# Performance work log

Hardware: AMD Instinct MI355X
Metric: run time of the kernel (lower is better)

## Reference

```python
import jax, jax.numpy as jnp
import numpy as np

B, L, DIN, D, H, NL, DFF = 4, 1024, 64, 512, 8, 3, 2048
DH = D // H
N_RBF = 8
LARGE_NEG, CLAMP = 10000.0, 20.0


def layernorm(x, g, b, eps=1e-5):
    m = x.mean(-1, keepdims=True)
    v = x.var(-1, keepdims=True)
    return (x - m) * jax.lax.rsqrt(v + eps) * g + b


def sinusoidal_pe(length, d):
    pos = np.arange(length, dtype=np.float32)[:, None]
    div = np.exp(np.arange(0, d, 2, dtype=np.float32) * (-np.log(10000.0) / d))
    pe = np.zeros((length, d), dtype=np.float32)
    pe[:, 0::2] = np.sin(pos * div)
    pe[:, 1::2] = np.cos(pos * div)
    return jnp.asarray(pe)


def rbf(v):
    centers = jnp.linspace(0.0, 1.0, N_RBF)
    widths = jnp.full((N_RBF,), 0.2)
    diff = (v[..., None] - centers) / (widths + 1e-6)
    return jnp.exp(-0.5 * diff * diff)


def setup_inputs() -> dict:
    key = jax.random.key(0)
    ks = jax.random.split(key, 40)
    g = lambda k, shape: (jax.random.normal(k, shape) * 0.02).astype(jnp.float32)
    feat_dim = D + 2 + 2 * N_RBF  # base PE + raw(2) + 2 RBFs
    inp = {
        "x": jax.random.normal(ks[0], (B, L, DIN), jnp.float32),
        "lengths": jax.random.randint(ks[1], (B,), L // 2, L + 1),
        "input_delay": jax.random.uniform(ks[2], (B,), jnp.float32),
        "c_local": jax.random.uniform(ks[3], (B, L), jnp.float32).at[:, 0].set(0.0),
        "c_sink": jax.random.uniform(ks[4], (B, L), jnp.float32),
        # input projection
        "in_w": g(ks[5], (D, DIN)), "in_b": jnp.zeros((D,)),
        # delay encoder: Linear(1,D) -> GELU -> Linear(D,D) -> LN
        "de_w1": g(ks[6], (D, 1)), "de_b1": jnp.zeros((D,)),
        "de_w2": g(ks[7], (D, D)), "de_b2": jnp.zeros((D,)),
        "de_ln_g": jnp.ones((D,)), "de_ln_b": jnp.zeros((D,)),
        # corr positional encoding
        "cpe_w": g(ks[8], (D, feat_dim)), "cpe_b": jnp.zeros((D,)),
        "cpe_ln_g": jnp.ones((D,)), "cpe_ln_b": jnp.zeros((D,)),
        "gain": jnp.float32(0.5),
        # bias params
        "alpha": jnp.float32(10.0), "beta": jnp.float32(10.0),
        "floor": jnp.float32(0.1), "gamma": jnp.float32(0.7),
        # per-layer stacks
        "inproj_w": g(ks[9], (NL, 3 * D, D)), "inproj_b": jnp.zeros((NL, 3 * D)),
        "outproj_w": g(ks[10], (NL, D, D)), "outproj_b": jnp.zeros((NL, D)),
        "ln1_g": jnp.ones((NL, D)), "ln1_b": jnp.zeros((NL, D)),
        "ln2_g": jnp.ones((NL, D)), "ln2_b": jnp.zeros((NL, D)),
        "ff_w1": g(ks[11], (NL, DFF, D)), "ff_b1": jnp.zeros((NL, DFF)),
        "ff_w2": g(ks[12], (NL, D, DFF)), "ff_b2": jnp.zeros((NL, D)),
        "out_ln_g": jnp.ones((D,)), "out_ln_b": jnp.zeros((D,)),
    }
    return inp


def _forward(x, input_delay, c_local, c_sink, in_w, in_b, de_w1, de_b1, de_w2, de_b2,
             de_ln_g, de_ln_b, cpe_w, cpe_b, cpe_ln_g, cpe_ln_b, gain, alpha, beta,
             floor, gamma, inproj_w, inproj_b, outproj_w, outproj_b, ln1_g, ln1_b,
             ln2_g, ln2_b, ff_w1, ff_b1, ff_w2, ff_b2, out_ln_g, out_ln_b, lengths):
    Bc, Lc, _ = x.shape
    mask = jnp.arange(Lc)[None, :] >= lengths[:, None]          # [B,L] True=pad

    # input projection
    h = x @ in_w.T + in_b

    # delay feature encoder
    e = input_delay[:, None] @ de_w1.T + de_b1
    e = jax.nn.gelu(e, approximate=False) @ de_w2.T + de_b2
    e = layernorm(e, de_ln_g, de_ln_b)
    h = h + e[:, None, :]

    # corr positional encoding (uses clamped correlations)
    cl = jnp.clip(c_local, 0.0, 1.0)
    cs = jnp.clip(c_sink, 0.0, 1.0)
    pe_base = jnp.broadcast_to(sinusoidal_pe(Lc, D)[None], (Bc, Lc, D))
    z = jnp.concatenate([pe_base, jnp.stack([cl, cs], -1), rbf(cl), rbf(cs)], axis=-1)
    pe = layernorm(z @ cpe_w.T + cpe_b, cpe_ln_g, cpe_ln_b)
    pe = gain * pe
    pe = jnp.where(mask[..., None], 0.0, pe)
    h = h + pe

    # neighbor-correlation attention bias [B,1,L,L] (identical across layers/heads)
    idx = jnp.arange(Lc)
    neigh = jnp.abs(idx[None, :] - idx[:, None]) == 1           # [L,L]
    c_edge = jnp.zeros((Bc, Lc, Lc), x.dtype)
    c_edge = c_edge.at[:, 1:, :-1].set(jnp.broadcast_to(c_local[:, 1:, None], (Bc, Lc - 1, Lc - 1)))
    c_edge = c_edge.at[:, :-1, 1:].set(jnp.broadcast_to(c_local[:, None, 1:], (Bc, Lc - 1, Lc - 1)))
    bias = alpha * jnp.where(neigh[None], c_edge, 0.0)
    bias = jnp.where(mask[:, :, None] | mask[:, None, :], 0.0, bias)

    # sink bias (row 0 only): floor + (1-floor)*(c_sink^gamma)
    c_remap = floor + (1.0 - floor) * jnp.power(cs + 1e-6, gamma)
    sink_row = beta * jnp.where(mask, 0.0, c_remap)             # [B,L]
    attn_bias = bias[:, None].at[:, :, 0, :].add(sink_row[:, None, :])  # [B,1,L,L]

    pad = mask[:, None, None, :].astype(x.dtype)                # [B,1,1,L]
    scale = 1.0 / (DH ** 0.5)

    for i in range(NL):
        hn = layernorm(h, ln1_g[i], ln1_b[i])
        qkv = hn @ inproj_w[i].T + inproj_b[i]                  # [B,L,3D]
        q, k, v = jnp.split(qkv, 3, axis=-1)
        q = q.reshape(Bc, Lc, H, DH).transpose(0, 2, 1, 3)      # [B,H,L,d]
        k = k.reshape(Bc, Lc, H, DH).transpose(0, 2, 1, 3)
        v = v.reshape(Bc, Lc, H, DH).transpose(0, 2, 1, 3)
        scores = jnp.einsum('bhqd,bhkd->bhqk', q, k) * scale + attn_bias
        scores = scores - LARGE_NEG * pad
        scores = scores - scores.max(axis=-1, keepdims=True)
        scores = jnp.clip(scores, -CLAMP, CLAMP)
        attn = jax.nn.softmax(scores, axis=-1)
        o = jnp.einsum('bhqk,bhkd->bhqd', attn, v)
        o = o.transpose(0, 2, 1, 3).reshape(Bc, Lc, D)
        h = h + (o @ outproj_w[i].T + outproj_b[i])
        hn2 = layernorm(h, ln2_g[i], ln2_b[i])
        ff = jax.nn.gelu(hn2 @ ff_w1[i].T + ff_b1[i], approximate=False)
        h = h + (ff @ ff_w2[i].T + ff_b2[i])

    return layernorm(h, out_ln_g, out_ln_b)


def reference(x, lengths, input_delay, c_local, c_sink, in_w, in_b, de_w1, de_b1,
              de_w2, de_b2, de_ln_g, de_ln_b, cpe_w, cpe_b, cpe_ln_g, cpe_ln_b, gain,
              alpha, beta, floor, gamma, inproj_w, inproj_b, outproj_w, outproj_b,
              ln1_g, ln1_b, ln2_g, ln2_b, ff_w1, ff_b1, ff_w2, ff_b2, out_ln_g, out_ln_b):
    return _forward(x, input_delay, c_local, c_sink, in_w, in_b, de_w1, de_b1, de_w2,
                    de_b2, de_ln_g, de_ln_b, cpe_w, cpe_b, cpe_ln_g, cpe_ln_b, gain,
                    alpha, beta, floor, gamma, inproj_w, inproj_b, outproj_w,
                    outproj_b, ln1_g, ln1_b, ln2_g, ln2_b, ff_w1, ff_b1, ff_w2, ff_b2,
                    out_ln_g, out_ln_b, lengths)
```

## Files before the change

kernel.cpp:

```cpp
#include <hip/hip_runtime.h>
#include <math.h>

#define BB 4
#define LL 1024
#define DIN 64
#define DD 512
#define HH 8
#define DH 64
#define NLAYER 3
#define DFF 2048
#define FEAT 530
#define FEATP 576
#define MM 4096

typedef float f32x4 __attribute__((ext_vector_type(4)));
typedef short s16x8 __attribute__((ext_vector_type(8)));

__device__ __forceinline__ unsigned short f2bf(float f) {
    unsigned int u = __float_as_uint(f);
    u += 0x7fffu + ((u >> 16) & 1u);
    return (unsigned short)(u >> 16);
}
__device__ __forceinline__ float bf2f(unsigned short u) {
    return __uint_as_float(((unsigned int)u) << 16);
}
__device__ __forceinline__ float gelu_exact(float x) {
    return 0.5f * x * (1.0f + erff(x * 0.7071067811865475f));
}
__device__ __forceinline__ float wave_reduce_sum(float v) {
    #pragma unroll
    for (int o = 32; o; o >>= 1) v += __shfl_down(v, o);
    return v;
}
__device__ __forceinline__ void gload16(const unsigned short* g, unsigned short* l) {
    __builtin_amdgcn_global_load_lds(
        (const __attribute__((address_space(1))) unsigned int*)g,
        (__attribute__((address_space(3))) unsigned int*)l, 16, 0, 0);
}
__device__ __forceinline__ void cvt16(const float* src, unsigned short* dst) {
    float4 f0 = ((const float4*)src)[0];
    float4 f1 = ((const float4*)src)[1];
    float4 f2 = ((const float4*)src)[2];
    float4 f3 = ((const float4*)src)[3];
    ushort4 o0, o1, o2, o3;
    o0.x = f2bf(f0.x); o0.y = f2bf(f0.y); o0.z = f2bf(f0.z); o0.w = f2bf(f0.w);
    o1.x = f2bf(f1.x); o1.y = f2bf(f1.y); o1.z = f2bf(f1.z); o1.w = f2bf(f1.w);
    o2.x = f2bf(f2.x); o2.y = f2bf(f2.y); o2.z = f2bf(f2.z); o2.w = f2bf(f2.w);
    o3.x = f2bf(f3.x); o3.y = f2bf(f3.y); o3.z = f2bf(f3.z); o3.w = f2bf(f3.w);
    ((ushort4*)dst)[0] = o0;
    ((ushort4*)dst)[1] = o1;
    ((ushort4*)dst)[2] = o2;
    ((ushort4*)dst)[3] = o3;
}

__global__ __launch_bounds__(256) void prologue_kernel(
    const float* __restrict__ c_local, const float* __restrict__ c_sink,
    const int* __restrict__ lengths,
    const float* __restrict__ beta_p, const float* __restrict__ floor_p,
    const float* __restrict__ gamma_p,
    unsigned short* __restrict__ Z, float* __restrict__ srow,
    const float* __restrict__ x, const float* __restrict__ in_w,
    const float* __restrict__ cpe_w,
    unsigned short* __restrict__ x_bf, unsigned short* __restrict__ w_in,
    unsigned short* __restrict__ w_cpe,
    const float* __restrict__ delay, const float* __restrict__ de_w1, const float* __restrict__ de_b1,
    const float* __restrict__ de_w2, const float* __restrict__ de_b2,
    const float* __restrict__ de_lng, const float* __restrict__ de_lnb,
    float* __restrict__ e)
{
    int blk = blockIdx.x;
    int t = threadIdx.x;

    if (blk < LL) {
        int l = blk;
        for (int d = t; d < DD; d += 256) {
            int i = d >> 1;
            float dv = expf((float)(2 * i) * (-0.017988946135618352f));
            float ang = (float)l * dv;
            unsigned short pv = f2bf((d & 1) ? cosf(ang) : sinf(ang));
            #pragma unroll
            for (int bb = 0; bb < 4; ++bb)
                Z[(size_t)(bb * LL + l) * FEATP + d] = pv;
        }
        {
            int bb = t >> 6, j = t & 63;
            float cl = c_local[(size_t)bb * LL + l]; cl = fminf(fmaxf(cl, 0.f), 1.f);
            float cs = c_sink [(size_t)bb * LL + l]; cs = fminf(fmaxf(cs, 0.f), 1.f);
            float v = 0.f;
            if (j == 0) v = cl;
            else if (j == 1) v = cs;
            else if (j < 10)  { float c = (float)(j - 2) * (1.0f / 7.0f);  float df = (cl - c) / 0.200001f; v = expf(-0.5f * df * df); }
            else if (j < 18)  { float c = (float)(j - 10) * (1.0f / 7.0f); float df = (cs - c) / 0.200001f; v = expf(-0.5f * df * df); }
            Z[(size_t)(bb * LL + l) * FEATP + 512 + j] = (j < 18) ? f2bf(v) : 0;
            if (j == 32) {
                float sv = (*beta_p) * ((*floor_p) + (1.f - (*floor_p)) * powf(cs + 1e-6f, *gamma_p));
                srow[bb * LL + l] = (l < lengths[bb]) ? sv : 0.f;
            }
        }
    } else if (blk < LL + 256) {
        const int N0s = MM * DIN;
        const int N1s = N0s + 512 * 64;
        const int NCHs = N1s / 16;
        int vb = blk - LL;
        for (int c = vb * 256 + t; c < NCHs; c += 256 * 256) {
            int i = c * 16;
            if (i < N0s) cvt16(x + i, x_bf + i);
            else         cvt16(in_w + (i - N0s), w_in + (i - N0s));
        }
        for (int j = vb * 256 + t; j < 512 * FEATP; j += 256 * 256) {
            int r = j / FEATP, c2 = j - r * FEATP;
            w_cpe[j] = (c2 < FEAT) ? f2bf(cpe_w[(size_t)r * FEAT + c2]) : 0;
        }
    } else {
        __shared__ float g1[DD];
        __shared__ float red[16];
        int b = blk - (LL + 256);
        float d0 = delay[b];
        g1[t]       = gelu_exact(d0 * de_w1[t]       + de_b1[t]);
        g1[t + 256] = gelu_exact(d0 * de_w1[t + 256] + de_b1[t + 256]);
        __syncthreads();
        float s0 = de_b2[t], s1 = de_b2[t + 256];
        const float* wr0 = de_w2 + (size_t)t * DD;
        const float* wr1 = de_w2 + (size_t)(t + 256) * DD;
        for (int j = 0; j < DD; j += 4) {
            float4 a4 = *(const float4*)(wr0 + j);
            float4 b4 = *(const float4*)(wr1 + j);
            float gj0 = g1[j], gj1 = g1[j+1], gj2 = g1[j+2], gj3 = g1[j+3];
            s0 += a4.x * gj0 + a4.y * gj1 + a4.z * gj2 + a4.w * gj3;
            s1 += b4.x * gj0 + b4.y * gj1 + b4.z * gj2 + b4.w * gj3;
        }
        float s = s0 + s1, ss = s0 * s0 + s1 * s1;
        float rs = wave_reduce_sum(s), rss = wave_reduce_sum(ss);
        int lane = t & 63, w = t >> 6;
        if (lane == 0) { red[w] = rs; red[8 + w] = rss; }
        __syncthreads();
        float mean = 0.f, msq = 0.f;
        #pragma unroll
        for (int i = 0; i < 4; ++i) { mean += red[i]; msq += red[8 + i]; }
        mean *= (1.0f / DD); msq *= (1.0f / DD);
        float rstd = rsqrtf(msq - mean * mean + 1e-5f);
        e[(size_t)b * DD + t]       = (s0 - mean) * rstd * de_lng[t]       + de_lnb[t];
        e[(size_t)b * DD + t + 256] = (s1 - mean) * rstd * de_lng[t + 256] + de_lnb[t + 256];
    }
}

template<int BM, int BN, int FM, int FN, int WGN>
__device__ __forceinline__ void gemm_body(
    const unsigned short* __restrict__ A, const unsigned short* __restrict__ W,
    const float* __restrict__ bias, const float* __restrict__ resid,
    float* __restrict__ outf, unsigned short* __restrict__ outb,
    int M, int N, int K, int mode, int bm, int bn,
    unsigned short* As, unsigned short* Ws)
{
    int t = threadIdx.x;
    int lane = t & 63, wid = t >> 6;
    int wr = wid / WGN, wc = wid % WGN;
    int l15 = lane & 15, lg = lane >> 4;
    int sr = lane >> 3;
    int sc = ((lane & 7) ^ sr) * 8;
    int ph0 = (lg ^ (l15 & 7)) * 8;
    int ph1 = ((lg + 4) ^ (l15 & 7)) * 8;

    f32x4 acc[FM][FN] = {};
    int nk = K >> 6;

    auto stage = [&](int buf, int ks) {
        int kb = ks * 64;
        #pragma unroll
        for (int i = 0; i < BM / 32; ++i) {
            int row = wid * (BM / 4) + i * 8 + sr;
            gload16(A + (size_t)(bm + row) * K + kb + sc, &As[(size_t)buf * BM * 64 + (wid * (BM / 4) + i * 8) * 64]);
        }
        #pragma unroll
        for (int i = 0; i < BN / 32; ++i) {
            int row = wid * (BN / 4) + i * 8 + sr;
            gload16(W + (size_t)(bn + row) * K + kb + sc, &Ws[(size_t)buf * BN * 64 + (wid * (BN / 4) + i * 8) * 64]);
        }
    };

    stage(0, 0);
    __syncthreads();

    int cur = 0;
    for (int ks = 0; ks < nk; ++ks) {
        if (ks + 1 < nk) stage(cur ^ 1, ks + 1);
        s16x8 af0[FM], af1[FM], wf0[FN], wf1[FN];
        #pragma unroll
        for (int mi = 0; mi < FM; ++mi) {
            int row = wr * FM * 16 + mi * 16 + l15;
            af0[mi] = *(const s16x8*)&As[(size_t)cur * BM * 64 + row * 64 + ph0];
            af1[mi] = *(const s16x8*)&As[(size_t)cur * BM * 64 + row * 64 + ph1];
        }
        #pragma unroll
        for (int ni = 0; ni < FN; ++ni) {
            int row = wc * FN * 16 + ni * 16 + l15;
            wf0[ni] = *(const s16x8*)&Ws[(size_t)cur * BN * 64 + row * 64 + ph0];
            wf1[ni] = *(const s16x8*)&Ws[(size_t)cur * BN * 64 + row * 64 + ph1];
        }
        #pragma unroll
        for (int mi = 0; mi < FM; ++mi)
            #pragma unroll
            for (int ni = 0; ni < FN; ++ni) {
                acc[mi][ni] = __builtin_amdgcn_mfma_f32_16x16x32_bf16(af0[mi], wf0[ni], acc[mi][ni], 0, 0, 0);
                acc[mi][ni] = __builtin_amdgcn_mfma_f32_16x16x32_bf16(af1[mi], wf1[ni], acc[mi][ni], 0, 0, 0);
            }
        __syncthreads();
        cur ^= 1;
    }

    int rbase = (lane >> 4) * 4;
    #pragma unroll
    for (int mi = 0; mi < FM; ++mi) {
        #pragma unroll
        for (int ni = 0; ni < FN; ++ni) {
            int n = bn + wc * FN * 16 + ni * 16 + l15;
            float bzc = (mode == 4) ? 0.f : bias[n];
            #pragma unroll
            for (int r2 = 0; r2 < 4; ++r2) {
                int m = bm + wr * FM * 16 + mi * 16 + rbase + r2;
                float v = acc[mi][ni][r2] + ((mode == 4) ? bias[m] : bzc);
                size_t o = (size_t)m * N + n;
                if (mode == 0)      outf[o] = v;
                else if (mode == 1) outb[o] = f2bf(v);
                else if (mode == 2) outf[o] = v + resid[o];
                else if (mode == 3) outb[o] = f2bf(gelu_exact(v));
                else                outb[o] = f2bf(v);
            }
        }
    }
}

template<int BM, int BN, int FM, int FN, int WGN, int MODE>
__global__ __launch_bounds__(256) void gemm_t(
    const unsigned short* __restrict__ A, const unsigned short* __restrict__ W,
    const float* __restrict__ bias, const float* __restrict__ resid,
    float* __restrict__ outf, unsigned short* __restrict__ outb,
    int M, int N, int K)
{
    __shared__ __align__(16) unsigned short As[2 * BM * 64];
    __shared__ __align__(16) unsigned short Ws[2 * BN * 64];
    gemm_body<BM, BN, FM, FN, WGN>(A, W, bias, resid, outf, outb, M, N, K, MODE,
                                   blockIdx.y * BM, blockIdx.x * BN, As, Ws);
}

__global__ __launch_bounds__(256) void gemm_pre_dual(
    const unsigned short* __restrict__ x_bf, const unsigned short* __restrict__ w_in,
    const float* __restrict__ in_b, float* __restrict__ h,
    const unsigned short* __restrict__ Zb, const unsigned short* __restrict__ w_cpe,
    const float* __restrict__ cpe_b, float* __restrict__ cpe_pre,
    const float* __restrict__ inproj_w, const float* __restrict__ outproj_w,
    const float* __restrict__ ff_w1, const float* __restrict__ ff_w2,
    unsigned short* __restrict__ w_inproj, unsigned short* __restrict__ w_outproj,
    unsigned short* __restrict__ w_ff1, unsigned short* __restrict__ w_ff2)
{
    __shared__ __align__(16) unsigned short As[2 * 64 * 64];
    __shared__ __align__(16) unsigned short Ws[2 * 64 * 64];
    int id = blockIdx.x;
    if (id < 512) {
        gemm_body<64, 64, 2, 2, 2>(x_bf, w_in, in_b, nullptr, h, nullptr,
                                   MM, DD, DIN, 0, (id >> 3) * 64, (id & 7) * 64, As, Ws);
    } else if (id < 1024) {
        id -= 512;
        gemm_body<64, 64, 2, 2, 2>(Zb, w_cpe, cpe_b, nullptr, cpe_pre, nullptr,
                                   MM, DD, FEATP, 0, (id >> 3) * 64, (id & 7) * 64, As, Ws);
    } else {
        const int B0 = 3 * 1536 * 512;
        const int B1 = B0 + 3 * 512 * 512;
        const int B2 = B1 + 3 * 2048 * 512;
        const int B3 = B2 + 3 * 512 * 2048;
        const int NCH = B3 / 16;
        int vb = id - 1024;
        int t = threadIdx.x;
        for (int c = vb * 256 + t; c < NCH; c += 1024 * 256) {
            int i = c * 16;
            if (i < B0)      cvt16(inproj_w + i,         w_inproj + i);
            else if (i < B1) cvt16(outproj_w + (i - B0), w_outproj + (i - B0));
            else if (i < B2) cvt16(ff_w1 + (i - B1),     w_ff1 + (i - B1));
            else             cvt16(ff_w2 + (i - B2),     w_ff2 + (i - B2));
        }
    }
}

__global__ __launch_bounds__(256) void gemm_qkv_dual(
    const unsigned short* __restrict__ act1,
    const unsigned short* __restrict__ wqk, const float* __restrict__ qk_bias,
    unsigned short* __restrict__ qkb,
    const unsigned short* __restrict__ wv, const float* __restrict__ v_bias,
    unsigned short* __restrict__ vtb)
{
    __shared__ __align__(16) unsigned short As[2 * 64 * 64];
    __shared__ __align__(16) unsigned short Ws[2 * 64 * 64];
    int id = blockIdx.x;
    if (id < 1024) {
        gemm_body<64, 64, 2, 2, 2>(act1, wqk, qk_bias, nullptr, nullptr, qkb,
                                   MM, 1024, DD, 1, (id >> 4) * 64, (id & 15) * 64, As, Ws);
    } else {
        id -= 1024;
        gemm_body<64, 64, 2, 2, 2>(wv, act1, v_bias, nullptr, nullptr, vtb,
                                   DD, MM, DD, 4, (id >> 6) * 64, (id & 63) * 64, As, Ws);
    }
}

#define SK 72
#define SPB 72
__global__ __launch_bounds__(256) void attn_mfma(
    const unsigned short* __restrict__ qk, const unsigned short* __restrict__ Vt,
    const float* __restrict__ c_local, const float* __restrict__ srow,
    const int* __restrict__ lengths,
    const float* __restrict__ alpha_p,
    unsigned short* __restrict__ o)
{
    __shared__ __align__(16) unsigned short Ks[2][64 * SK];
    __shared__ __align__(16) unsigned short Vts[2][64 * SK];
    __shared__ __align__(16) unsigned short Psb[64 * SPB];

    int id = blockIdx.x;
    int q0 = (id & 15) * 64;
    int hh = (id >> 4) & 7;
    int b  = id >> 7;

    int t  = threadIdx.x;
    int lane = t & 63, w = t >> 6;
    int l15 = lane & 15, lg = lane >> 4;
    int len = lengths[b];
    int nt = (len + 63) >> 6;
    int kt0 = q0 >> 6;
    bool sink_blk = (q0 == 0);
    const float alpha = *alpha_p;

    const unsigned short* qrow = qk + (size_t)(b * LL + q0 + w * 16 + l15) * 1024 + hh * DH;
    s16x8 qf0 = *(const s16x8*)(qrow + lg * 8);
    s16x8 qf1 = *(const s16x8*)(qrow + 32 + lg * 8);
    #pragma unroll
    for (int j = 0; j < 8; ++j) {
        qf0[j] = (short)f2bf(bf2f((unsigned short)qf0[j]) * 0.125f);
        qf1[j] = (short)f2bf(bf2f((unsigned short)qf1[j]) * 0.125f);
    }

    float cm1[4], cp1[4];
    #pragma unroll
    for (int r2 = 0; r2 < 4; ++r2) {
        int qi = q0 + w * 16 + lg * 4 + r2;
        cm1[r2] = 0.f; cp1[r2] = 0.f;
        if (qi >= 1 && qi < len) {
            int src = (qi == 1 || qi == LL - 1) ? qi : qi - 1;
            cm1[r2] = alpha * c_local[(size_t)b * LL + src];
        }
        if (qi + 1 < LL && qi < len)
            cp1[r2] = alpha * c_local[(size_t)b * LL + qi + 1];
    }
    bool need_sink = (sink_blk && w == 0 && lg == 0);

    float m_run[4], l_run[4];
    f32x4 accO[4] = {};
    #pragma unroll
    for (int r2 = 0; r2 < 4; ++r2) { m_run[r2] = -1e30f; l_run[r2] = 0.f; }

    int sr = t >> 3, sc8 = (t & 7) * 8;
    const unsigned short* kbase = qk + (size_t)(b * LL) * 1024 + 512 + hh * DH;
    const unsigned short* vbase = Vt + (size_t)(hh * DH) * MM + b * LL;

    uint4 pk0 = *(const uint4*)(kbase + (size_t)sr * 1024 + sc8);
    uint4 pk1 = *(const uint4*)(kbase + (size_t)(sr + 32) * 1024 + sc8);
    uint4 pv0 = *(const uint4*)(vbase + (size_t)sr * MM + sc8);
    uint4 pv1 = *(const uint4*)(vbase + (size_t)(sr + 32) * MM + sc8);
    *(uint4*)&Ks[0][sr * SK + sc8]         = pk0;
    *(uint4*)&Ks[0][(sr + 32) * SK + sc8]  = pk1;
    *(uint4*)&Vts[0][sr * SK + sc8]        = pv0;
    *(uint4*)&Vts[0][(sr + 32) * SK + sc8] = pv1;
    __syncthreads();

    int cur = 0;
    for (int kt = 0; kt < nt; ++kt) {
        int k0 = kt * 64;
        bool pre = (kt + 1 < nt);
        if (pre) {
            int kn = k0 + 64;
            pk0 = *(const uint4*)(kbase + (size_t)(kn + sr) * 1024 + sc8);
            pk1 = *(const uint4*)(kbase + (size_t)(kn + sr + 32) * 1024 + sc8);
            pv0 = *(const uint4*)(vbase + (size_t)sr * MM + kn + sc8);
            pv1 = *(const uint4*)(vbase + (size_t)(sr + 32) * MM + kn + sc8);
        }

        f32x4 accS[4] = {};
        #pragma unroll
        for (int ct = 0; ct < 4; ++ct) {
            s16x8 kf0 = *(const s16x8*)&Ks[cur][(ct * 16 + l15) * SK + lg * 8];
            s16x8 kf1 = *(const s16x8*)&Ks[cur][(ct * 16 + l15) * SK + 32 + lg * 8];
            accS[ct] = __builtin_amdgcn_mfma_f32_16x16x32_bf16(qf0, kf0, accS[ct], 0, 0, 0);
            accS[ct] = __builtin_amdgcn_mfma_f32_16x16x32_bf16(qf1, kf1, accS[ct], 0, 0, 0);
        }

        float m4[4] = { -1e30f, -1e30f, -1e30f, -1e30f };
        bool slow = sink_blk || (kt >= kt0 - 1 && kt <= kt0 + 1) || (k0 + 64 > len);
        if (!slow) {
            #pragma unroll
            for (int ct = 0; ct < 4; ++ct)
                #pragma unroll
                for (int r2 = 0; r2 < 4; ++r2)
                    m4[r2] = fmaxf(m4[r2], accS[ct][r2]);
        } else if (k0 + 64 <= len) {
            #pragma unroll
            for (int ct = 0; ct < 4; ++ct) {
                int k = k0 + ct * 16 + l15;
                float sink_ct = need_sink ? srow[(size_t)b * LL + k] : 0.f;
                #pragma unroll
                for (int r2 = 0; r2 < 4; ++r2) {
                    int qi = q0 + w * 16 + lg * 4 + r2;
                    float v = accS[ct][r2];
                    if (k == qi - 1) v += cm1[r2];
                    else if (k == qi + 1) v += cp1[r2];
                    if (r2 == 0) v += sink_ct;
                    accS[ct][r2] = v;
                    m4[r2] = fmaxf(m4[r2], v);
                }
            }
        } else {
            #pragma unroll
            for (int ct = 0; ct < 4; ++ct) {
                int k = k0 + ct * 16 + l15;
                bool maskk = (k >= len);
                float sink_ct = need_sink ? srow[(size_t)b * LL + k] : 0.f;
                #pragma unroll
                for (int r2 = 0; r2 < 4; ++r2) {
                    int qi = q0 + w * 16 + lg * 4 + r2;
                    float v = accS[ct][r2];
                    if (k == qi - 1) v += cm1[r2];
                    else if (k == qi + 1 && !maskk) v += cp1[r2];
                    if (r2 == 0) v += sink_ct;
                    if (maskk) v -= 10000.f;
                    accS[ct][r2] = v;
                    m4[r2] = fmaxf(m4[r2], v);
                }
            }
        }

        #pragma unroll
        for (int r2 = 0; r2 < 4; ++r2) {
            #pragma unroll
            for (int msk = 1; msk < 16; msk <<= 1) m4[r2] = fmaxf(m4[r2], __shfl_xor(m4[r2], msk));
            float mnew = fmaxf(m_run[r2], m4[r2]);
            float scl = __expf(m_run[r2] - mnew);
            m_run[r2] = mnew;
            float rowsum = 0.f;
            #pragma unroll
            for (int ct = 0; ct < 4; ++ct) {
                float p = __expf(accS[ct][r2] - mnew);
                rowsum += p;
                Psb[(w * 16 + lg * 4 + r2) * SPB + ct * 16 + l15] = f2bf(p);
            }
            #pragma unroll
            for (int msk = 1; msk < 16; msk <<= 1) rowsum += __shfl_xor(rowsum, msk);
            l_run[r2] = l_run[r2] * scl + rowsum;
            #pragma unroll
            for (int dt = 0; dt < 4; ++dt) accO[dt][r2] *= scl;
        }

        #pragma unroll
        for (int kk = 0; kk < 2; ++kk) {
            s16x8 pf = *(const s16x8*)&Psb[(w * 16 + l15) * SPB + kk * 32 + lg * 8];
            #pragma unroll
            for (int dt = 0; dt < 4; ++dt) {
                s16x8 vf = *(const s16x8*)&Vts[cur][(dt * 16 + l15) * SK + kk * 32 + lg * 8];
                accO[dt] = __builtin_amdgcn_mfma_f32_16x16x32_bf16(pf, vf, accO[dt], 0, 0, 0);
            }
        }

        if (pre) {
            int nxt = cur ^ 1;
            *(uint4*)&Ks[nxt][sr * SK + sc8]         = pk0;
            *(uint4*)&Ks[nxt][(sr + 32) * SK + sc8]  = pk1;
            *(uint4*)&Vts[nxt][sr * SK + sc8]        = pv0;
            *(uint4*)&Vts[nxt][(sr + 32) * SK + sc8] = pv1;
        }
        __syncthreads();
        cur ^= 1;
    }

    #pragma unroll
    for (int r2 = 0; r2 < 4; ++r2) {
        float inv = 1.f / l_run[r2];
        int qi = q0 + w * 16 + lg * 4 + r2;
        #pragma unroll
        for (int dt = 0; dt < 4; ++dt)
            o[(size_t)(b * LL + qi) * DD + hh * DH + dt * 16 + l15] = f2bf(accO[dt][r2] * inv);
    }
}

__global__ __launch_bounds__(256) void embed_ep_kernel(
    const float* __restrict__ cpe_pre, const float* __restrict__ e,
    const int* __restrict__ lengths,
    const float* __restrict__ cpe_g, const float* __restrict__ cpe_lb,
    const float* __restrict__ gain_p, float* __restrict__ h)
{
    int row = blockIdx.x;
    int b = row >> 10, l = row & 1023;
    int t = threadIdx.x;
    __shared__ float red[16];
    const float* cp = cpe_pre + (size_t)row * DD;
    float v0 = cp[t], v1 = cp[t + 256];
    float s = v0 + v1, ss = v0 * v0 + v1 * v1;
    float rs = wave_reduce_sum(s), rss = wave_reduce_sum(ss);
    int lane = t & 63, w = t >> 6;
    if (lane == 0) { red[w] = rs; red[8 + w] = rss; }
    __syncthreads();
    float mean = 0.f, msq = 0.f;
    #pragma unroll
    for (int i = 0; i < 4; ++i) { mean += red[i]; msq += red[8 + i]; }
    mean *= (1.0f / DD); msq *= (1.0f / DD);
    float rstd = rsqrtf(msq - mean * mean + 1e-5f);
    bool maskp = (l >= lengths[b]);
    float gain = *gain_p;
    float pe0 = maskp ? 0.f : gain * ((v0 - mean) * rstd * cpe_g[t] + cpe_lb[t]);
    float pe1 = maskp ? 0.f : gain * ((v1 - mean) * rstd * cpe_g[t + 256] + cpe_lb[t + 256]);
    h[(size_t)row * DD + t]       += e[(size_t)b * DD + t] + pe0;
    h[(size_t)row * DD + t + 256] += e[(size_t)b * DD + t + 256] + pe1;
}

__global__ __launch_bounds__(256) void ln_kernel(
    const float* __restrict__ in, float* __restrict__ out,
    const float* __restrict__ g, const float* __restrict__ bta)
{
    int row = blockIdx.x; int t = threadIdx.x;
    __shared__ float red[16];
    const float* xr = in + (size_t)row * DD;
    float2 v = ((const float2*)xr)[t];
    float s = v.x + v.y, ss = v.x * v.x + v.y * v.y;
    float rs = wave_reduce_sum(s), rss = wave_reduce_sum(ss);
    int lane = t & 63, w = t >> 6;
    if (lane == 0) { red[w] = rs; red[8 + w] = rss; }
    __syncthreads();
    float mean = 0.f, msq = 0.f;
    #pragma unroll
    for (int i = 0; i < 4; ++i) { mean += red[i]; msq += red[8 + i]; }
    mean *= (1.0f / DD); msq *= (1.0f / DD);
    float rstd = rsqrtf(msq - mean * mean + 1e-5f);
    float2 gg = ((const float2*)g)[t], bb = ((const float2*)bta)[t];
    float2 o;
    o.x = (v.x - mean) * rstd * gg.x + bb.x;
    o.y = (v.y - mean) * rstd * gg.y + bb.y;
    ((float2*)(out + (size_t)row * DD))[t] = o;
}

__global__ __launch_bounds__(256) void ln_bf16_kernel(
    const float* __restrict__ in, unsigned short* __restrict__ out,
    const float* __restrict__ g, const float* __restrict__ bta)
{
    int row = blockIdx.x; int t = threadIdx.x;
    __shared__ float red[16];
    const float* xr = in + (size_t)row * DD;
    float2 v = ((const float2*)xr)[t];
    float s = v.x + v.y, ss = v.x * v.x + v.y * v.y;
    float rs = wave_reduce_sum(s), rss = wave_reduce_sum(ss);
    int lane = t & 63, w = t >> 6;
    if (lane == 0) { red[w] = rs; red[8 + w] = rss; }
    __syncthreads();
    float mean = 0.f, msq = 0.f;
    #pragma unroll
    for (int i = 0; i < 4; ++i) { mean += red[i]; msq += red[8 + i]; }
    mean *= (1.0f / DD); msq *= (1.0f / DD);
    float rstd = rsqrtf(msq - mean * mean + 1e-5f);
    float2 gg = ((const float2*)g)[t], bb = ((const float2*)bta)[t];
    ushort2 o;
    o.x = f2bf((v.x - mean) * rstd * gg.x + bb.x);
    o.y = f2bf((v.y - mean) * rstd * gg.y + bb.y);
    ((ushort2*)(out + (size_t)row * DD))[t] = o;
}

extern "C" void kernel_launch(void* const* d_in, const int* in_sizes, int n_in,
                              void* d_out, int out_size, void* d_ws, size_t ws_size,
                              hipStream_t stream)
{
    const float* x          = (const float*)d_in[0];
    const int*   lengths    = (const int*)  d_in[1];
    const float* input_delay= (const float*)d_in[2];
    const float* c_local    = (const float*)d_in[3];
    const float* c_sink     = (const float*)d_in[4];
    const float* in_w       = (const float*)d_in[5];
    const float* in_b       = (const float*)d_in[6];
    const float* de_w1      = (const float*)d_in[7];
    const float* de_b1      = (const float*)d_in[8];
    const float* de_w2      = (const float*)d_in[9];
    const float* de_b2      = (const float*)d_in[10];
    const float* de_ln_g    = (const float*)d_in[11];
    const float* de_ln_b    = (const float*)d_in[12];
    const float* cpe_w      = (const float*)d_in[13];
    const float* cpe_b      = (const float*)d_in[14];
    const float* cpe_ln_g   = (const float*)d_in[15];
    const float* cpe_ln_b   = (const float*)d_in[16];
    const float* gain       = (const float*)d_in[17];
    const float* alpha      = (const float*)d_in[18];
    const float* beta       = (const float*)d_in[19];
    const float* floorp     = (const float*)d_in[20];
    const float* gammap     = (const float*)d_in[21];
    const float* inproj_w   = (const float*)d_in[22];
    const float* inproj_b   = (const float*)d_in[23];
    const float* outproj_w  = (const float*)d_in[24];
    const float* outproj_b  = (const float*)d_in[25];
    const float* ln1_g      = (const float*)d_in[26];
    const float* ln1_b      = (const float*)d_in[27];
    const float* ln2_g      = (const float*)d_in[28];
    const float* ln2_b      = (const float*)d_in[29];
    const float* ff_w1      = (const float*)d_in[30];
    const float* ff_b1      = (const float*)d_in[31];
    const float* ff_w2      = (const float*)d_in[32];
    const float* ff_b2      = (const float*)d_in[33];
    const float* out_ln_g   = (const float*)d_in[34];
    const float* out_ln_b   = (const float*)d_in[35];

    char* base = (char*)d_ws;
    float* h            = (float*)base;
    unsigned short* act1 = (unsigned short*)(base + 8u*1024*1024);
    char* bigb          = base + 12u*1024*1024;
    unsigned short* qkb  = (unsigned short*)bigb;
    unsigned short* vtb  = (unsigned short*)(bigb + 12u*1024*1024);
    unsigned short* ffb  = (unsigned short*)bigb;
    unsigned short* Zb   = (unsigned short*)bigb;
    unsigned short* x_bf = (unsigned short*)(bigb + 5u*1024*1024);
    float* cpe_pre       = (float*)(bigb + 8u*1024*1024);
    unsigned short* w_inproj  = (unsigned short*)(base + 28u*1024*1024);
    unsigned short* w_outproj = w_inproj  + (size_t)3*1536*512;
    unsigned short* w_ff1     = w_outproj + (size_t)3*512*512;
    unsigned short* w_ff2     = w_ff1     + (size_t)3*2048*512;
    unsigned short* w_in      = w_ff2     + (size_t)3*512*2048;
    unsigned short* w_cpe     = w_in      + (size_t)512*64;
    float* e                  = (float*)(w_cpe + (size_t)512*FEATP);
    float* srow               = e + (size_t)BB*DD;

    prologue_kernel<<<LL + 256 + BB, 256, 0, stream>>>(
        c_local, c_sink, lengths, beta, floorp, gammap, Zb, srow,
        x, in_w, cpe_w, x_bf, w_in, w_cpe,
        input_delay, de_w1, de_b1, de_w2, de_b2, de_ln_g, de_ln_b, e);

    gemm_pre_dual<<<2048, 256, 0, stream>>>(x_bf, w_in, in_b, h, Zb, w_cpe, cpe_b, cpe_pre,
                                            inproj_w, outproj_w, ff_w1, ff_w2,
                                            w_inproj, w_outproj, w_ff1, w_ff2);
    embed_ep_kernel<<<MM, 256, 0, stream>>>(cpe_pre, e, lengths, cpe_ln_g, cpe_ln_b, gain, h);

    for (int i = 0; i < NLAYER; ++i) {
        const unsigned short* wqk = w_inproj + (size_t)i * 1536 * 512;
        const unsigned short* wv  = wqk + (size_t)1024 * 512;
        ln_bf16_kernel<<<MM, 256, 0, stream>>>(h, act1, ln1_g + (size_t)i * DD, ln1_b + (size_t)i * DD);
        gemm_qkv_dual<<<1536, 256, 0, stream>>>(act1, wqk, inproj_b + (size_t)i * 1536,
                                                qkb, wv, inproj_b + (size_t)i * 1536 + 1024, vtb);
        attn_mfma<<<512, 256, 0, stream>>>(qkb, vtb, c_local, srow, lengths, alpha, act1);
        gemm_t<64, 64, 2, 2, 2, 2><<<dim3(DD / 64, MM / 64), 256, 0, stream>>>(
            act1, w_outproj + (size_t)i * 512 * 512, outproj_b + (size_t)i * DD,
            h, h, nullptr, MM, DD, DD);
        ln_bf16_kernel<<<MM, 256, 0, stream>>>(h, act1, ln2_g + (size_t)i * DD, ln2_b + (size_t)i * DD);
        gemm_t<128, 128, 4, 4, 2, 3><<<dim3(DFF / 128, MM / 128), 256, 0, stream>>>(
            act1, w_ff1 + (size_t)i * 2048 * 512, ff_b1 + (size_t)i * DFF,
            nullptr, nullptr, ffb, MM, DFF, DD);
        gemm_t<64, 64, 2, 2, 2, 2><<<dim3(DD / 64, MM / 64), 256, 0, stream>>>(
            ffb, w_ff2 + (size_t)i * 512 * 2048, ff_b2 + (size_t)i * DD,
            h, h, nullptr, MM, DD, DFF);
    }
    ln_kernel<<<MM, 256, 0, stream>>>(h, (float*)d_out, out_ln_g, out_ln_b);
}
```

Before: 425.7 us.

## Split delay-encoder matvec across 64 blocks and defer its layernorm to embed kernel

The delay-encoder second linear layer was computed by only 4 blocks, each doing a 512x512 matvec serially, which could become a tail on the prologue kernel. It is now split over 64 blocks, each computing 32 output rows, with 8 threads per row combined by shuffle reduction. Its layernorm moves into embed_ep_kernel, which recomputes the per-batch statistics in every row block. That adds a small amount of redundant reduction work across 4096 blocks in exchange for a shorter prologue critical path.

Result: faster. 394.9 us (-7.2%).

```diff
diff --git a/kernel.cpp b/kernel.cpp
--- a/kernel.cpp
+++ b/kernel.cpp
@@ -65,8 +65,7 @@
     unsigned short* __restrict__ w_cpe,
     const float* __restrict__ delay, const float* __restrict__ de_w1, const float* __restrict__ de_b1,
     const float* __restrict__ de_w2, const float* __restrict__ de_b2,
-    const float* __restrict__ de_lng, const float* __restrict__ de_lnb,
-    float* __restrict__ e)
+    float* __restrict__ e_pre)
 {
     int blk = blockIdx.x;
     int t = threadIdx.x;
@@ -113,34 +112,26 @@
         }
     } else {
         __shared__ float g1[DD];
-        __shared__ float red[16];
-        int b = blk - (LL + 256);
+        int idx = blk - (LL + 256);
+        int b  = idx >> 4;
+        int r0 = (idx & 15) * 32;
         float d0 = delay[b];
         g1[t]       = gelu_exact(d0 * de_w1[t]       + de_b1[t]);
         g1[t + 256] = gelu_exact(d0 * de_w1[t + 256] + de_b1[t + 256]);
         __syncthreads();
-        float s0 = de_b2[t], s1 = de_b2[t + 256];
-        const float* wr0 = de_w2 + (size_t)t * DD;
-        const float* wr1 = de_w2 + (size_t)(t + 256) * DD;
-        for (int j = 0; j < DD; j += 4) {
-            float4 a4 = *(const float4*)(wr0 + j);
-            float4 b4 = *(const float4*)(wr1 + j);
-            float gj0 = g1[j], gj1 = g1[j+1], gj2 = g1[j+2], gj3 = g1[j+3];
-            s0 += a4.x * gj0 + a4.y * gj1 + a4.z * gj2 + a4.w * gj3;
-            s1 += b4.x * gj0 + b4.y * gj1 + b4.z * gj2 + b4.w * gj3;
-        }
-        float s = s0 + s1, ss = s0 * s0 + s1 * s1;
-        float rs = wave_reduce_sum(s), rss = wave_reduce_sum(ss);
-        int lane = t & 63, w = t >> 6;
-        if (lane == 0) { red[w] = rs; red[8 + w] = rss; }
-        __syncthreads();
-        float mean = 0.f, msq = 0.f;
-        #pragma unroll
-        for (int i = 0; i < 4; ++i) { mean += red[i]; msq += red[8 + i]; }
-        mean *= (1.0f / DD); msq *= (1.0f / DD);
-        float rstd = rsqrtf(msq - mean * mean + 1e-5f);
-        e[(size_t)b * DD + t]       = (s0 - mean) * rstd * de_lng[t]       + de_lnb[t];
-        e[(size_t)b * DD + t + 256] = (s1 - mean) * rstd * de_lng[t + 256] + de_lnb[t + 256];
+        int r = t >> 3, c = t & 7;
+        const float* wr = de_w2 + (size_t)(r0 + r) * DD + c * 64;
+        const float* gc = g1 + c * 64;
+        float s = 0.f;
+        #pragma unroll
+        for (int j = 0; j < 64; j += 4) {
+            float4 a4 = *(const float4*)(wr + j);
+            s += a4.x * gc[j] + a4.y * gc[j+1] + a4.z * gc[j+2] + a4.w * gc[j+3];
+        }
+        s += __shfl_xor(s, 1);
+        s += __shfl_xor(s, 2);
+        s += __shfl_xor(s, 4);
+        if (c == 0) e_pre[(size_t)b * DD + r0 + r] = s + de_b2[r0 + r];
     }
 }
 
@@ -488,33 +479,44 @@
 }
 
 __global__ __launch_bounds__(256) void embed_ep_kernel(
-    const float* __restrict__ cpe_pre, const float* __restrict__ e,
+    const float* __restrict__ cpe_pre, const float* __restrict__ e_pre,
     const int* __restrict__ lengths,
     const float* __restrict__ cpe_g, const float* __restrict__ cpe_lb,
+    const float* __restrict__ de_lng, const float* __restrict__ de_lnb,
     const float* __restrict__ gain_p, float* __restrict__ h)
 {
     int row = blockIdx.x;
     int b = row >> 10, l = row & 1023;
     int t = threadIdx.x;
-    __shared__ float red[16];
+    __shared__ float red[32];
     const float* cp = cpe_pre + (size_t)row * DD;
     float v0 = cp[t], v1 = cp[t + 256];
-    float s = v0 + v1, ss = v0 * v0 + v1 * v1;
-    float rs = wave_reduce_sum(s), rss = wave_reduce_sum(ss);
+    float e0 = e_pre[(size_t)b * DD + t], e1 = e_pre[(size_t)b * DD + t + 256];
+    float s  = v0 + v1, ss  = v0 * v0 + v1 * v1;
+    float s2 = e0 + e1, ss2 = e0 * e0 + e1 * e1;
+    float rs  = wave_reduce_sum(s),  rss  = wave_reduce_sum(ss);
+    float rs2 = wave_reduce_sum(s2), rss2 = wave_reduce_sum(ss2);
     int lane = t & 63, w = t >> 6;
-    if (lane == 0) { red[w] = rs; red[8 + w] = rss; }
+    if (lane == 0) { red[w] = rs; red[8 + w] = rss; red[16 + w] = rs2; red[24 + w] = rss2; }
     __syncthreads();
-    float mean = 0.f, msq = 0.f;
-    #pragma unroll
-    for (int i = 0; i < 4; ++i) { mean += red[i]; msq += red[8 + i]; }
+    float mean = 0.f, msq = 0.f, mean_e = 0.f, msq_e = 0.f;
+    #pragma unroll
+    for (int i = 0; i < 4; ++i) {
+        mean += red[i]; msq += red[8 + i];
+        mean_e += red[16 + i]; msq_e += red[24 + i];
+    }
     mean *= (1.0f / DD); msq *= (1.0f / DD);
-    float rstd = rsqrtf(msq - mean * mean + 1e-5f);
+    mean_e *= (1.0f / DD); msq_e *= (1.0f / DD);
+    float rstd   = rsqrtf(msq - mean * mean + 1e-5f);
+    float rstd_e = rsqrtf(msq_e - mean_e * mean_e + 1e-5f);
+    float eln0 = (e0 - mean_e) * rstd_e * de_lng[t]       + de_lnb[t];
+    float eln1 = (e1 - mean_e) * rstd_e * de_lng[t + 256] + de_lnb[t + 256];
     bool maskp = (l >= lengths[b]);
     float gain = *gain_p;
     float pe0 = maskp ? 0.f : gain * ((v0 - mean) * rstd * cpe_g[t] + cpe_lb[t]);
     float pe1 = maskp ? 0.f : gain * ((v1 - mean) * rstd * cpe_g[t + 256] + cpe_lb[t + 256]);
-    h[(size_t)row * DD + t]       += e[(size_t)b * DD + t] + pe0;
-    h[(size_t)row * DD + t + 256] += e[(size_t)b * DD + t + 256] + pe1;
+    h[(size_t)row * DD + t]       += eln0 + pe0;
+    h[(size_t)row * DD + t + 256] += eln1 + pe1;
 }
 
 __global__ __launch_bounds__(256) void ln_kernel(
@@ -624,18 +626,19 @@
     unsigned short* w_ff2     = w_ff1     + (size_t)3*2048*512;
     unsigned short* w_in      = w_ff2     + (size_t)3*512*2048;
     unsigned short* w_cpe     = w_in      + (size_t)512*64;
-    float* e                  = (float*)(w_cpe + (size_t)512*FEATP);
-    float* srow               = e + (size_t)BB*DD;
-
-    prologue_kernel<<<LL + 256 + BB, 256, 0, stream>>>(
+    float* e_pre              = (float*)(w_cpe + (size_t)512*FEATP);
+    float* srow               = e_pre + (size_t)BB*DD;
+
+    prologue_kernel<<<LL + 256 + 64, 256, 0, stream>>>(
         c_local, c_sink, lengths, beta, floorp, gammap, Zb, srow,
         x, in_w, cpe_w, x_bf, w_in, w_cpe,
-        input_delay, de_w1, de_b1, de_w2, de_b2, de_ln_g, de_ln_b, e);
+        input_delay, de_w1, de_b1, de_w2, de_b2, e_pre);
 
     gemm_pre_dual<<<2048, 256, 0, stream>>>(x_bf, w_in, in_b, h, Zb, w_cpe, cpe_b, cpe_pre,
                                             inproj_w, outproj_w, ff_w1, ff_w2,
                                             w_inproj, w_outproj, w_ff1, w_ff2);
-    embed_ep_kernel<<<MM, 256, 0, stream>>>(cpe_pre, e, lengths, cpe_ln_g, cpe_ln_b, gain, h);
+    embed_ep_kernel<<<MM, 256, 0, stream>>>(cpe_pre, e_pre, lengths, cpe_ln_g, cpe_ln_b,
+                                            de_ln_g, de_ln_b, gain, h);
 
     for (int i = 0; i < NLAYER; ++i) {
         const unsigned short* wqk = w_inproj + (size_t)i * 1536 * 512;
```
